# Kernel tuning notes

Hardware: AMD Instinct MI355X
Metric: run time of the kernel (lower is better)

## Reference

```python
import jax, jax.numpy as jnp
import numpy as np

E = 1024  # hidden_size
H = 16    # num_heads
D = E // H  # head_dim = 64


def setup_inputs() -> dict:
    key = jax.random.key(0)
    ks = jax.random.split(key, 10)
    s = 1.0 / np.sqrt(E)
    inp = {
        "hidden_states": jax.random.normal(ks[0], (2, 2048, E), dtype=jnp.float32),
        "attention_mask": jnp.ones((2, 2048), dtype=jnp.float32),
        "Wq": jax.random.normal(ks[1], (E, E), dtype=jnp.float32) * s,
        "bq": jnp.zeros((E,), dtype=jnp.float32),
        "Wk": jax.random.normal(ks[2], (E, E), dtype=jnp.float32) * s,
        "bk": jnp.zeros((E,), dtype=jnp.float32),
        "Wv": jax.random.normal(ks[3], (E, E), dtype=jnp.float32) * s,
        "bv": jnp.zeros((E,), dtype=jnp.float32),
        "Wo": jax.random.normal(ks[4], (E, E), dtype=jnp.float32) * s,
        "bo": jnp.zeros((E,), dtype=jnp.float32),
    }
    return inp


def _split_heads(x):
    # [B, S, E] -> [B, H, S, D]
    b, s, _ = x.shape
    return x.reshape(b, s, H, D).transpose(0, 2, 1, 3)


def reference(hidden_states, attention_mask, Wq, bq, Wk, bk, Wv, bv, Wo, bo):
    b, s, _ = hidden_states.shape
    q = _split_heads(hidden_states @ Wq + bq)  # [B,H,S,D]
    k = _split_heads(hidden_states @ Wk + bk)
    v = _split_heads(hidden_states @ Wv + bv)
    scores = jnp.einsum('bhqd,bhkd->bhqk', q, k) / jnp.sqrt(jnp.float32(D))
    scores = scores + (1.0 - attention_mask)[:, None, None, :] * -10000.0
    probs = jax.nn.softmax(scores, axis=-1)
    ctx = jnp.einsum('bhqk,bhkd->bhqd', probs, v)  # [B,H,S,D]
    ctx = ctx.transpose(0, 2, 1, 3).reshape(b, s, E)
    return ctx @ Wo + bo
```

## Files before the change

kernel.cpp:

```cpp
#include <hip/hip_runtime.h>
#include <hip/hip_bf16.h>
#include <stdint.h>

typedef __bf16 bf16x8 __attribute__((ext_vector_type(8)));
typedef __bf16 bf16x4_t __attribute__((ext_vector_type(4)));
typedef float  f32x4  __attribute__((ext_vector_type(4)));
typedef short  short8 __attribute__((ext_vector_type(8)));
typedef short  short4v __attribute__((ext_vector_type(4)));
typedef float  float4v __attribute__((ext_vector_type(4)));

#define AS1 __attribute__((address_space(1)))
#define AS3 __attribute__((address_space(3)))

__device__ __forceinline__ void g2l16(const void* g, void* l) {
    __builtin_amdgcn_global_load_lds((const AS1 void*)g, (AS3 void*)l, 16, 0, 0);
}

__device__ __forceinline__ short f2bf(float f) {
    unsigned u = __builtin_bit_cast(unsigned, f);
    unsigned r = u + 0x7FFFu + ((u >> 16) & 1u);
    return (short)(r >> 16);
}

__device__ __forceinline__ bf16x8 ldb8(const short* p) {
    return __builtin_bit_cast(bf16x8, *(const short8*)p);
}

__device__ __forceinline__ float fast_exp2(float x) {
    return __builtin_amdgcn_exp2f(x);
}

#define LOG2E 1.44269504f
#define QSCL (0.125f * LOG2E)

__global__ __launch_bounds__(256) void prep(
    const float* __restrict__ X, short* __restrict__ Xb,
    const float* __restrict__ W0, const float* __restrict__ W1,
    const float* __restrict__ W2, const float* __restrict__ W3,
    short* __restrict__ T0, short* __restrict__ T1,
    short* __restrict__ T2, short* __restrict__ T3) {
    int gb = blockIdx.x;
    if (gb < 4096) {
        int i = (gb * 256 + threadIdx.x) * 4;
        float4v v = *(const float4v*)(X + i);
        short4v o;
        o[0] = f2bf(v[0]); o[1] = f2bf(v[1]); o[2] = f2bf(v[2]); o[3] = f2bf(v[3]);
        *(short4v*)(Xb + i) = o;
        return;
    }
    int t = gb - 4096;
    int z = t >> 10, rem = t & 1023;
    int xb = rem & 31, yb = rem >> 5;
    const float* W = z == 0 ? W0 : z == 1 ? W1 : z == 2 ? W2 : W3;
    short* T = z == 0 ? T0 : z == 1 ? T1 : z == 2 ? T2 : T3;
    __shared__ float tt[32][33];
    int n0 = xb * 32, k0 = yb * 32;
    int tx = threadIdx.x & 31, ty = threadIdx.x >> 5;
#pragma unroll
    for (int i = 0; i < 4; i++)
        tt[ty + i * 8][tx] = W[(size_t)(k0 + ty + i * 8) * 1024 + n0 + tx];
    __syncthreads();
#pragma unroll
    for (int i = 0; i < 4; i++)
        T[(size_t)(n0 + ty + i * 8) * 1024 + k0 + tx] = f2bf(tt[tx][ty + i * 8]);
}

#define VROW 136
__global__ __launch_bounds__(256) void gemm_qkv(
    const short* __restrict__ Xb,
    const short* __restrict__ WqT, const short* __restrict__ WkT, const short* __restrict__ WvT,
    const float* __restrict__ bq, const float* __restrict__ bk, const float* __restrict__ bv,
    short* __restrict__ Qb, short* __restrict__ Kb, short* __restrict__ VT) {
    const int K = 1024, N = 1024;
    int mt = blockIdx.x;
    int yy = blockIdx.y;
    int mat = yy >> 3, nt = yy & 7;
    const short* Bt = mat == 0 ? WqT : mat == 1 ? WkT : WvT;
    const float* bias = mat == 0 ? bq : mat == 1 ? bk : bv;

    int tid = threadIdx.x;
    int w = tid >> 6, lane = tid & 63;
    int quad = lane >> 4, l16 = lane & 15;
    int wy = w >> 1, wx = w & 1;

    __shared__ __align__(16) short smem[128 * VROW];
    short* A_lds = smem;
    short* B_lds = smem + 4096;

    f32x4 acc[4][4];
#pragma unroll
    for (int i = 0; i < 4; i++)
#pragma unroll
        for (int j = 0; j < 4; j++) acc[i][j] = (f32x4){0.f, 0.f, 0.f, 0.f};

    int m0 = mt * 128, n0 = nt * 128;

    if (mat < 2) {
        for (int kt = 0; kt < 32; kt++) {
            __syncthreads();
#pragma unroll
            for (int c = 0; c < 2; c++) {
                int row = w * 32 + c * 16 + (lane >> 2);
                g2l16(Xb + (size_t)(m0 + row) * K + kt * 32 + (lane & 3) * 8,
                      &A_lds[(w * 32 + c * 16) * 32]);
                g2l16(Bt + (size_t)(n0 + row) * K + kt * 32 + (lane & 3) * 8,
                      &B_lds[(w * 32 + c * 16) * 32]);
            }
            __syncthreads();
            bf16x8 af[4], bfr[4];
#pragma unroll
            for (int i = 0; i < 4; i++) {
                af[i]  = ldb8(&A_lds[(wy * 64 + i * 16 + l16) * 32 + quad * 8]);
                bfr[i] = ldb8(&B_lds[(wx * 64 + i * 16 + l16) * 32 + quad * 8]);
            }
#pragma unroll
            for (int ni = 0; ni < 4; ni++)
#pragma unroll
                for (int mi = 0; mi < 4; mi++)
                    acc[ni][mi] = __builtin_amdgcn_mfma_f32_16x16x32_bf16(bfr[ni], af[mi], acc[ni][mi], 0, 0, 0);
        }
        short* Cout = mat == 0 ? Qb : Kb;
        float s = mat == 0 ? QSCL : 1.0f;
#pragma unroll
        for (int ni = 0; ni < 4; ni++) {
            int c0 = n0 + wx * 64 + ni * 16 + quad * 4;
            float4v bv4 = *(const float4v*)(bias + c0);
#pragma unroll
            for (int mi = 0; mi < 4; mi++) {
                int row = m0 + wy * 64 + mi * 16 + l16;
                f32x4 a = acc[ni][mi];
                f32x4 av = {(a[0] + bv4[0]) * s, (a[1] + bv4[1]) * s,
                            (a[2] + bv4[2]) * s, (a[3] + bv4[3]) * s};
                bf16x4_t ob = __builtin_convertvector(av, bf16x4_t);
                *(short4v*)&Cout[(size_t)row * N + c0] = __builtin_bit_cast(short4v, ob);
            }
        }
    } else {
        for (int kt = 0; kt < 32; kt++) {
            __syncthreads();
#pragma unroll
            for (int c = 0; c < 2; c++) {
                int row = w * 32 + c * 16 + (lane >> 2);
                g2l16(Xb + (size_t)(m0 + row) * K + kt * 32 + (lane & 3) * 8,
                      &A_lds[(w * 32 + c * 16) * 32]);
                g2l16(Bt + (size_t)(n0 + row) * K + kt * 32 + (lane & 3) * 8,
                      &B_lds[(w * 32 + c * 16) * 32]);
            }
            __syncthreads();
            bf16x8 af[4], bfr[4];
#pragma unroll
            for (int i = 0; i < 4; i++) {
                af[i]  = ldb8(&A_lds[(wy * 64 + i * 16 + l16) * 32 + quad * 8]);
                bfr[i] = ldb8(&B_lds[(wx * 64 + i * 16 + l16) * 32 + quad * 8]);
            }
#pragma unroll
            for (int mi = 0; mi < 4; mi++)
#pragma unroll
                for (int ni = 0; ni < 4; ni++)
                    acc[mi][ni] = __builtin_amdgcn_mfma_f32_16x16x32_bf16(af[mi], bfr[ni], acc[mi][ni], 0, 0, 0);
        }
        __syncthreads();
#pragma unroll
        for (int ni = 0; ni < 4; ni++) {
            int cl = wx * 64 + ni * 16 + l16;
            float bv_ = bias[n0 + cl];
#pragma unroll
            for (int mi = 0; mi < 4; mi++) {
                int ml = wy * 64 + mi * 16 + quad * 4;
                f32x4 a = acc[mi][ni];
                f32x4 av = {a[0] + bv_, a[1] + bv_, a[2] + bv_, a[3] + bv_};
                bf16x4_t ob = __builtin_convertvector(av, bf16x4_t);
                *(short4v*)&smem[cl * VROW + ml] = __builtin_bit_cast(short4v, ob);
            }
        }
        __syncthreads();
        int bb = m0 >> 11, ss0 = m0 & 2047;
        int t16 = tid & 15, cw = tid >> 4;
#pragma unroll
        for (int p = 0; p < 8; p++) {
            int cl = p * 16 + cw;
            int col = n0 + cl;
            *(short8*)&VT[(((size_t)(bb * 16)) << 17) + (size_t)col * 2048 + ss0 + t16 * 8] =
                *(const short8*)&smem[cl * VROW + t16 * 8];
        }
    }
}

__global__ __launch_bounds__(256) void gemm_out(
    const short* __restrict__ Ab, const short* __restrict__ Bt,
    const float* __restrict__ bias, float* __restrict__ C) {
    const int K = 1024, N = 1024;
    int mt = blockIdx.x, nt = blockIdx.y;
    int tid = threadIdx.x;
    int w = tid >> 6, lane = tid & 63;
    int quad = lane >> 4, l16 = lane & 15;

    __shared__ __align__(16) short A_lds[64 * 32];
    __shared__ __align__(16) short B_lds[128 * 32];

    f32x4 acc[2][4];
#pragma unroll
    for (int ni = 0; ni < 2; ni++)
#pragma unroll
        for (int mi = 0; mi < 4; mi++) acc[ni][mi] = (f32x4){0.f, 0.f, 0.f, 0.f};

    int m0 = mt * 64, n0 = nt * 128;
    for (int kt = 0; kt < 32; kt++) {
        __syncthreads();
        {
            int row = w * 16 + (lane >> 2);
            g2l16(Ab + (size_t)(m0 + row) * K + kt * 32 + (lane & 3) * 8,
                  &A_lds[(w * 16) * 32]);
        }
#pragma unroll
        for (int c = 0; c < 2; c++) {
            int row = w * 32 + c * 16 + (lane >> 2);
            g2l16(Bt + (size_t)(n0 + row) * K + kt * 32 + (lane & 3) * 8,
                  &B_lds[(w * 32 + c * 16) * 32]);
        }
        __syncthreads();
        bf16x8 af[4], bfr[2];
#pragma unroll
        for (int i = 0; i < 4; i++)
            af[i] = ldb8(&A_lds[(i * 16 + l16) * 32 + quad * 8]);
#pragma unroll
        for (int i = 0; i < 2; i++)
            bfr[i] = ldb8(&B_lds[(w * 32 + i * 16 + l16) * 32 + quad * 8]);
#pragma unroll
        for (int ni = 0; ni < 2; ni++)
#pragma unroll
            for (int mi = 0; mi < 4; mi++)
                acc[ni][mi] = __builtin_amdgcn_mfma_f32_16x16x32_bf16(bfr[ni], af[mi], acc[ni][mi], 0, 0, 0);
    }
#pragma unroll
    for (int ni = 0; ni < 2; ni++) {
        int c0 = n0 + w * 32 + ni * 16 + quad * 4;
        float4v bv4 = *(const float4v*)(bias + c0);
#pragma unroll
        for (int mi = 0; mi < 4; mi++) {
            int row = m0 + mi * 16 + l16;
            f32x4 a = acc[ni][mi];
            float4v av = {a[0] + bv4[0], a[1] + bv4[1], a[2] + bv4[2], a[3] + bv4[3]};
            *(float4v*)&C[(size_t)row * N + c0] = av;
        }
    }
}

#define PROW 72
__global__ __launch_bounds__(512) void attn_kernel(
    const short* __restrict__ Qb, const short* __restrict__ Kb,
    const short* __restrict__ VT, const float* __restrict__ mask,
    short* __restrict__ ctx) {
    const int S = 2048, E = 1024, HH = 16;
    int g = blockIdx.x;
    int p = (g & 7) + 8 * (g >> 7);
    int qb = (g >> 3) & 15;
    int b = p >> 4, h = p & 15;

    int tid = threadIdx.x;
    int w = tid >> 6, lane = tid & 63;
    int quad = lane >> 4, l16 = lane & 15;

    __shared__ __align__(16) short K_lds[2][64 * 64];
    __shared__ __align__(16) short VT_lds[2][64 * 64];
    __shared__ __align__(16) short P_lds[8][16 * PROW];
    __shared__ int maskflag;

    if (tid == 0) maskflag = 1;
    __syncthreads();
    {
        float4v m = *(const float4v*)(mask + b * S + tid * 4);
        if (!(m[0] == 1.f && m[1] == 1.f && m[2] == 1.f && m[3] == 1.f))
            maskflag = 0;
    }
    __syncthreads();
    const bool nomask = (maskflag != 0);

    int q0 = qb * 128;

    bf16x8 qf[2];
#pragma unroll
    for (int kc = 0; kc < 2; kc++)
        qf[kc] = ldb8(Qb + (size_t)(b * S + q0 + w * 16 + l16) * E + h * 64 + kc * 32 + quad * 8);

    short8 ones_s = {0x3F80, 0x3F80, 0x3F80, 0x3F80, 0x3F80, 0x3F80, 0x3F80, 0x3F80};
    bf16x8 vones = __builtin_bit_cast(bf16x8, ones_s);

    f32x4 O_t[4];
    f32x4 lacc = (f32x4){0.f, 0.f, 0.f, 0.f};
#pragma unroll
    for (int nd = 0; nd < 4; nd++) O_t[nd] = (f32x4){0.f, 0.f, 0.f, 0.f};

    const short* Kbase = Kb + (size_t)b * S * E + h * 64;
    const short* Vbase = VT + (size_t)(b * HH + h) * 64 * S;
    short* Pw = &P_lds[w][0];
    int rsw = l16 & 7;

    int srow = w * 8 + (lane >> 3);
    int ssrcb = (lane & 7) ^ (srow & 7);

    g2l16(Kbase + (size_t)srow * E + ssrcb * 8, &K_lds[0][(w * 8) * 64]);
    g2l16(Vbase + (size_t)srow * S + 0 + ssrcb * 8, &VT_lds[0][(w * 8) * 64]);
    __syncthreads();

    for (int kt = 0; kt < 32; kt++) {
        int cur = kt & 1;
        int k0 = kt * 64;
        if (kt < 31) {
            int k1 = k0 + 64;
            g2l16(Kbase + (size_t)(k1 + srow) * E + ssrcb * 8, &K_lds[cur ^ 1][(w * 8) * 64]);
            g2l16(Vbase + (size_t)srow * S + k1 + ssrcb * 8, &VT_lds[cur ^ 1][(w * 8) * 64]);
        }
        const short* Kl = &K_lds[cur][0];
        const short* Vl = &VT_lds[cur][0];

        f32x4 sc[4];
#pragma unroll
        for (int ni = 0; ni < 4; ni++) sc[ni] = (f32x4){0.f, 0.f, 0.f, 0.f};
#pragma unroll
        for (int ni = 0; ni < 4; ni++) {
#pragma unroll
            for (int kc = 0; kc < 2; kc++) {
                int blk = (kc * 4 + quad) ^ rsw;
                bf16x8 kf = ldb8(&Kl[(ni * 16 + l16) * 64 + blk * 8]);
                sc[ni] = __builtin_amdgcn_mfma_f32_16x16x32_bf16(kf, qf[kc], sc[ni], 0, 0, 0);
            }
        }

        if (!nomask) {
#pragma unroll
            for (int ni = 0; ni < 4; ni++) {
                float4v mrow = *(const float4v*)(mask + b * S + k0 + ni * 16 + quad * 4);
#pragma unroll
                for (int r = 0; r < 4; r++)
                    sc[ni][r] += (1.0f - mrow[r]) * (-10000.0f * LOG2E);
            }
        }

#pragma unroll
        for (int ni = 0; ni < 4; ni++)
#pragma unroll
            for (int r = 0; r < 4; r++)
                sc[ni][r] = fast_exp2(sc[ni][r]);

#pragma unroll
        for (int ni = 0; ni < 4; ni++) {
            bf16x4_t pb = __builtin_convertvector(sc[ni], bf16x4_t);
            *(short4v*)&Pw[l16 * PROW + ni * 16 + quad * 4] =
                __builtin_bit_cast(short4v, pb);
        }

#pragma unroll
        for (int ks = 0; ks < 2; ks++) {
            bf16x8 pf = ldb8(&Pw[l16 * PROW + ks * 32 + quad * 8]);
            lacc = __builtin_amdgcn_mfma_f32_16x16x32_bf16(vones, pf, lacc, 0, 0, 0);
#pragma unroll
            for (int nd = 0; nd < 4; nd++) {
                int blk = (ks * 4 + quad) ^ rsw;
                bf16x8 vf = ldb8(&Vl[(nd * 16 + l16) * 64 + blk * 8]);
                O_t[nd] = __builtin_amdgcn_mfma_f32_16x16x32_bf16(vf, pf, O_t[nd], 0, 0, 0);
            }
        }
        __syncthreads();
    }

    {
        float l = lacc[0];
        float inv = l > 0.f ? 1.0f / l : 0.f;
        int row = q0 + w * 16 + l16;
#pragma unroll
        for (int nd = 0; nd < 4; nd++) {
            f32x4 o = O_t[nd];
            f32x4 os = {o[0] * inv, o[1] * inv, o[2] * inv, o[3] * inv};
            bf16x4_t ob = __builtin_convertvector(os, bf16x4_t);
            *(short4v*)&ctx[(size_t)(b * S + row) * E + h * 64 + nd * 16 + quad * 4] =
                __builtin_bit_cast(short4v, ob);
        }
    }
}

extern "C" void kernel_launch(void* const* d_in, const int* in_sizes, int n_in,
                              void* d_out, int out_size, void* d_ws, size_t ws_size,
                              hipStream_t stream) {
    const float* X    = (const float*)d_in[0];
    const float* mask = (const float*)d_in[1];
    const float* Wq   = (const float*)d_in[2];
    const float* bq   = (const float*)d_in[3];
    const float* Wk   = (const float*)d_in[4];
    const float* bk   = (const float*)d_in[5];
    const float* Wv   = (const float*)d_in[6];
    const float* bv   = (const float*)d_in[7];
    const float* Wo   = (const float*)d_in[8];
    const float* bo   = (const float*)d_in[9];
    float* out = (float*)d_out;

    char* ws = (char*)d_ws;
    short* Xb  = (short*)(ws);
    short* WqT = (short*)(ws + (8u << 20));
    short* WkT = (short*)(ws + (10u << 20));
    short* WvT = (short*)(ws + (12u << 20));
    short* WoT = (short*)(ws + (14u << 20));
    short* Qb  = (short*)(ws + (16u << 20));
    short* Kb  = (short*)(ws + (24u << 20));
    short* VT  = (short*)(ws + (32u << 20));
    short* ctx = Xb;

    prep<<<8192, 256, 0, stream>>>(X, Xb, Wq, Wk, Wv, Wo, WqT, WkT, WvT, WoT);
    gemm_qkv<<<dim3(32, 24), 256, 0, stream>>>(Xb, WqT, WkT, WvT, bq, bk, bv, Qb, Kb, VT);
    attn_kernel<<<512, 512, 0, stream>>>(Qb, Kb, VT, mask, ctx);
    gemm_out<<<dim3(64, 8), 256, 0, stream>>>(ctx, WoT, bo, out);
}
```

Baseline: 194.0 us.

## Give each attention wave two query sub-tiles to reuse K/V fragments

The attention kernel drops from 8 to 4 waves per block, and each wave now handles 32 query rows as two 16-row sub-tiles. Every K and V fragment read from shared memory feeds two MFMAs instead of one, which halves LDS fragment traffic per unit of work. The trade-offs are higher register pressure and fewer waves per block to hide latency. The P buffer row pitch changes to 76, so P is reread with two 8-byte loads, and the mask check and tile loads are rewritten for 256 threads.

```diff
diff --git a/kernel.cpp b/kernel.cpp
--- a/kernel.cpp
+++ b/kernel.cpp
@@ -246,8 +246,8 @@
     }
 }
 
-#define PROW 72
-__global__ __launch_bounds__(512) void attn_kernel(
+#define PROW 76
+__global__ __launch_bounds__(256) void attn_kernel(
     const short* __restrict__ Qb, const short* __restrict__ Kb,
     const short* __restrict__ VT, const float* __restrict__ mask,
     short* __restrict__ ctx) {
@@ -263,14 +263,16 @@
 
     __shared__ __align__(16) short K_lds[2][64 * 64];
     __shared__ __align__(16) short VT_lds[2][64 * 64];
-    __shared__ __align__(16) short P_lds[8][16 * PROW];
+    __shared__ __align__(16) short P_lds[4][32 * PROW];
     __shared__ int maskflag;
 
     if (tid == 0) maskflag = 1;
     __syncthreads();
     {
-        float4v m = *(const float4v*)(mask + b * S + tid * 4);
-        if (!(m[0] == 1.f && m[1] == 1.f && m[2] == 1.f && m[3] == 1.f))
+        float4v m0v = *(const float4v*)(mask + b * S + tid * 8);
+        float4v m1v = *(const float4v*)(mask + b * S + tid * 8 + 4);
+        if (!(m0v[0] == 1.f && m0v[1] == 1.f && m0v[2] == 1.f && m0v[3] == 1.f &&
+              m1v[0] == 1.f && m1v[1] == 1.f && m1v[2] == 1.f && m1v[3] == 1.f))
             maskflag = 0;
     }
     __syncthreads();
@@ -278,29 +280,39 @@
 
     int q0 = qb * 128;
 
-    bf16x8 qf[2];
-#pragma unroll
-    for (int kc = 0; kc < 2; kc++)
-        qf[kc] = ldb8(Qb + (size_t)(b * S + q0 + w * 16 + l16) * E + h * 64 + kc * 32 + quad * 8);
+    bf16x8 qf[2][2];
+#pragma unroll
+    for (int mi = 0; mi < 2; mi++)
+#pragma unroll
+        for (int kc = 0; kc < 2; kc++)
+            qf[mi][kc] = ldb8(Qb + (size_t)(b * S + q0 + w * 32 + mi * 16 + l16) * E + h * 64 + kc * 32 + quad * 8);
 
     short8 ones_s = {0x3F80, 0x3F80, 0x3F80, 0x3F80, 0x3F80, 0x3F80, 0x3F80, 0x3F80};
     bf16x8 vones = __builtin_bit_cast(bf16x8, ones_s);
 
-    f32x4 O_t[4];
-    f32x4 lacc = (f32x4){0.f, 0.f, 0.f, 0.f};
-#pragma unroll
-    for (int nd = 0; nd < 4; nd++) O_t[nd] = (f32x4){0.f, 0.f, 0.f, 0.f};
+    f32x4 O_t[2][4];
+    f32x4 lacc[2];
+#pragma unroll
+    for (int mi = 0; mi < 2; mi++) {
+        lacc[mi] = (f32x4){0.f, 0.f, 0.f, 0.f};
+#pragma unroll
+        for (int nd = 0; nd < 4; nd++) O_t[mi][nd] = (f32x4){0.f, 0.f, 0.f, 0.f};
+    }
 
     const short* Kbase = Kb + (size_t)b * S * E + h * 64;
     const short* Vbase = VT + (size_t)(b * HH + h) * 64 * S;
     short* Pw = &P_lds[w][0];
     int rsw = l16 & 7;
 
-    int srow = w * 8 + (lane >> 3);
-    int ssrcb = (lane & 7) ^ (srow & 7);
-
-    g2l16(Kbase + (size_t)srow * E + ssrcb * 8, &K_lds[0][(w * 8) * 64]);
-    g2l16(Vbase + (size_t)srow * S + 0 + ssrcb * 8, &VT_lds[0][(w * 8) * 64]);
+    int sr8 = lane >> 3;
+    int ssrcb = (lane & 7) ^ sr8;
+
+#pragma unroll
+    for (int c = 0; c < 2; c++) {
+        int row = w * 16 + c * 8 + sr8;
+        g2l16(Kbase + (size_t)row * E + ssrcb * 8, &K_lds[0][(w * 16 + c * 8) * 64]);
+        g2l16(Vbase + (size_t)row * S + 0 + ssrcb * 8, &VT_lds[0][(w * 16 + c * 8) * 64]);
+    }
     __syncthreads();
 
     for (int kt = 0; kt < 32; kt++) {
@@ -308,22 +320,30 @@
         int k0 = kt * 64;
         if (kt < 31) {
             int k1 = k0 + 64;
-            g2l16(Kbase + (size_t)(k1 + srow) * E + ssrcb * 8, &K_lds[cur ^ 1][(w * 8) * 64]);
-            g2l16(Vbase + (size_t)srow * S + k1 + ssrcb * 8, &VT_lds[cur ^ 1][(w * 8) * 64]);
+#pragma unroll
+            for (int c = 0; c < 2; c++) {
+                int row = w * 16 + c * 8 + sr8;
+                g2l16(Kbase + (size_t)(k1 + row) * E + ssrcb * 8, &K_lds[cur ^ 1][(w * 16 + c * 8) * 64]);
+                g2l16(Vbase + (size_t)row * S + k1 + ssrcb * 8, &VT_lds[cur ^ 1][(w * 16 + c * 8) * 64]);
+            }
         }
         const short* Kl = &K_lds[cur][0];
         const short* Vl = &VT_lds[cur][0];
 
-        f32x4 sc[4];
-#pragma unroll
-        for (int ni = 0; ni < 4; ni++) sc[ni] = (f32x4){0.f, 0.f, 0.f, 0.f};
+        f32x4 sc[2][4];
+#pragma unroll
+        for (int mi = 0; mi < 2; mi++)
+#pragma unroll
+            for (int ni = 0; ni < 4; ni++) sc[mi][ni] = (f32x4){0.f, 0.f, 0.f, 0.f};
 #pragma unroll
         for (int ni = 0; ni < 4; ni++) {
 #pragma unroll
             for (int kc = 0; kc < 2; kc++) {
                 int blk = (kc * 4 + quad) ^ rsw;
                 bf16x8 kf = ldb8(&Kl[(ni * 16 + l16) * 64 + blk * 8]);
-                sc[ni] = __builtin_amdgcn_mfma_f32_16x16x32_bf16(kf, qf[kc], sc[ni], 0, 0, 0);
+#pragma unroll
+                for (int mi = 0; mi < 2; mi++)
+                    sc[mi][ni] = __builtin_amdgcn_mfma_f32_16x16x32_bf16(kf, qf[mi][kc], sc[mi][ni], 0, 0, 0);
             }
         }
 
@@ -332,45 +352,62 @@
             for (int ni = 0; ni < 4; ni++) {
                 float4v mrow = *(const float4v*)(mask + b * S + k0 + ni * 16 + quad * 4);
 #pragma unroll
+                for (int r = 0; r < 4; r++) {
+                    float madd = (1.0f - mrow[r]) * (-10000.0f * LOG2E);
+                    sc[0][ni][r] += madd;
+                    sc[1][ni][r] += madd;
+                }
+            }
+        }
+
+#pragma unroll
+        for (int mi = 0; mi < 2; mi++)
+#pragma unroll
+            for (int ni = 0; ni < 4; ni++)
+#pragma unroll
                 for (int r = 0; r < 4; r++)
-                    sc[ni][r] += (1.0f - mrow[r]) * (-10000.0f * LOG2E);
-            }
-        }
-
-#pragma unroll
-        for (int ni = 0; ni < 4; ni++)
-#pragma unroll
-            for (int r = 0; r < 4; r++)
-                sc[ni][r] = fast_exp2(sc[ni][r]);
-
-#pragma unroll
-        for (int ni = 0; ni < 4; ni++) {
-            bf16x4_t pb = __builtin_convertvector(sc[ni], bf16x4_t);
-            *(short4v*)&Pw[l16 * PROW + ni * 16 + quad * 4] =
-                __builtin_bit_cast(short4v, pb);
-        }
+                    sc[mi][ni][r] = fast_exp2(sc[mi][ni][r]);
+
+#pragma unroll
+        for (int mi = 0; mi < 2; mi++)
+#pragma unroll
+            for (int ni = 0; ni < 4; ni++) {
+                bf16x4_t pb = __builtin_convertvector(sc[mi][ni], bf16x4_t);
+                *(short4v*)&Pw[(mi * 16 + l16) * PROW + ni * 16 + quad * 4] =
+                    __builtin_bit_cast(short4v, pb);
+            }
 
 #pragma unroll
         for (int ks = 0; ks < 2; ks++) {
-            bf16x8 pf = ldb8(&Pw[l16 * PROW + ks * 32 + quad * 8]);
-            lacc = __builtin_amdgcn_mfma_f32_16x16x32_bf16(vones, pf, lacc, 0, 0, 0);
+            bf16x8 pf[2];
+#pragma unroll
+            for (int mi = 0; mi < 2; mi++) {
+                short4v p0 = *(const short4v*)&Pw[(mi * 16 + l16) * PROW + ks * 32 + quad * 8];
+                short4v p1 = *(const short4v*)&Pw[(mi * 16 + l16) * PROW + ks * 32 + quad * 8 + 4];
+                short8 pc = {p0[0], p0[1], p0[2], p0[3], p1[0], p1[1], p1[2], p1[3]};
+                pf[mi] = __builtin_bit_cast(bf16x8, pc);
+                lacc[mi] = __builtin_amdgcn_mfma_f32_16x16x32_bf16(vones, pf[mi], lacc[mi], 0, 0, 0);
+            }
 #pragma unroll
             for (int nd = 0; nd < 4; nd++) {
                 int blk = (ks * 4 + quad) ^ rsw;
                 bf16x8 vf = ldb8(&Vl[(nd * 16 + l16) * 64 + blk * 8]);
-                O_t[nd] = __builtin_amdgcn_mfma_f32_16x16x32_bf16(vf, pf, O_t[nd], 0, 0, 0);
+#pragma unroll
+                for (int mi = 0; mi < 2; mi++)
+                    O_t[mi][nd] = __builtin_amdgcn_mfma_f32_16x16x32_bf16(vf, pf[mi], O_t[mi][nd], 0, 0, 0);
             }
         }
         __syncthreads();
     }
 
-    {
-        float l = lacc[0];
+#pragma unroll
+    for (int mi = 0; mi < 2; mi++) {
+        float l = lacc[mi][0];
         float inv = l > 0.f ? 1.0f / l : 0.f;
-        int row = q0 + w * 16 + l16;
+        int row = q0 + w * 32 + mi * 16 + l16;
 #pragma unroll
         for (int nd = 0; nd < 4; nd++) {
-            f32x4 o = O_t[nd];
+            f32x4 o = O_t[mi][nd];
             f32x4 os = {o[0] * inv, o[1] * inv, o[2] * inv, o[3] * inv};
             bf16x4_t ob = __builtin_convertvector(os, bf16x4_t);
             *(short4v*)&ctx[(size_t)(b * S + row) * E + h * 64 + nd * 16 + quad * 4] =
@@ -407,6 +444,6 @@
 
     prep<<<8192, 256, 0, stream>>>(X, Xb, Wq, Wk, Wv, Wo, WqT, WkT, WvT, WoT);
     gemm_qkv<<<dim3(32, 24), 256, 0, stream>>>(Xb, WqT, WkT, WvT, bq, bk, bv, Qb, Kb, VT);
-    attn_kernel<<<512, 512, 0, stream>>>(Qb, Kb, VT, mask, ctx);
+    attn_kernel<<<512, 256, 0, stream>>>(Qb, Kb, VT, mask, ctx);
     gemm_out<<<dim3(64, 8), 256, 0, stream>>>(ctx, WoT, bo, out);
 }
```

New measurement: 200.4 us. 3.3% more time.
